# Kernel optimization log

Measured on AMD Instinct MI355X. Metric: run time of the kernel, lower is better.

Reference implementation:

```python
import jax, jax.numpy as jnp
import numpy as np

B, N, C = 1, 50000, 128
E, D = 800000, 2


def setup_inputs() -> dict:
    key = jax.random.key(0)
    k1, k2, k3 = jax.random.split(key, 3)
    x = jax.random.normal(k1, (B, N, C), dtype=jnp.float32)
    edge_weights = jax.random.normal(k2, (B, E, D), dtype=jnp.float32)
    directed_edges = jax.random.randint(k3, (B, E, 2), 0, N, dtype=jnp.int64)
    return {"x": x, "edge_weights": edge_weights, "directed_edges": directed_edges}


def reference(x, edge_weights, directed_edges):
    # x: [B, N, C] node features; edge_weights: [B, E, D]; directed_edges: [B, E, 2] = (target, source)
    b, n, c = x.shape
    _, e, d = edge_weights.shape
    target = directed_edges[..., 0]  # [B, E]
    source = directed_edges[..., 1]  # [B, E]
    bidx = jnp.arange(b)[:, None]  # [B, 1] broadcasts against [B, E]
    # gather node diffs per edge: [B, E, C]
    diff = x[bidx, source] - x[bidx, target]
    # weight by edge direction vector and flatten (C, D) -> C*D, matching torch reshape order
    message = jnp.einsum('bed,bec->becd', edge_weights, diff).reshape(b, e, c * d)
    # scatter-add into per-node gradient accumulator: [B, N, C*D]
    out = jnp.zeros((b, n, c * d), dtype=message.dtype)
    out = out.at[bidx, target].add(message)
    return out
```

## Files before the change

kernel.cpp:

```cpp
#include <hip/hip_runtime.h>


#define CAP 32
#define OVF_CAP 65536

typedef unsigned short u16;
typedef unsigned int u32;

__device__ __forceinline__ u16 f2bf(float f) {
  u32 u = __float_as_uint(f);
  return (u16)((u + 0x7FFFu + ((u >> 16) & 1u)) >> 16);
}
__device__ __forceinline__ float bf2f(u16 v) {
  return __uint_as_float(((u32)v) << 16);
}

__global__ __launch_bounds__(256) void k_cvt(const float* __restrict__ x,
                                             u16* __restrict__ xb, int total4) {
  const int stride = gridDim.x * blockDim.x;
  for (int i = blockIdx.x * blockDim.x + threadIdx.x; i < total4; i += stride) {
    const float4 v = reinterpret_cast<const float4*>(x)[i];
    ushort4 o;
    o.x = f2bf(v.x); o.y = f2bf(v.y); o.z = f2bf(v.z); o.w = f2bf(v.w);
    reinterpret_cast<ushort4*>(xb)[i] = o;
  }
}

__device__ __forceinline__ void append_one(int tgt, int src, float wx, float wy,
                                           int* counts, int4* rec,
                                           int* ovfcnt, int4* ovflist) {
  const int pos = atomicAdd(&counts[tgt], 1);
  if (pos < CAP) {
    int4 r;
    r.x = src; r.y = __float_as_int(wx); r.z = __float_as_int(wy); r.w = 0;
    rec[(size_t)tgt * CAP + pos] = r;
  } else {
    const int op = atomicAdd(ovfcnt, 1);
    if (op < OVF_CAP) {
      int4 r;
      r.x = tgt; r.y = src; r.z = __float_as_int(wx); r.w = __float_as_int(wy);
      ovflist[op] = r;
    }
  }
}

__global__ __launch_bounds__(256) void k_append(const int* __restrict__ edges,
                                                const float* __restrict__ ew,
                                                int* __restrict__ counts,
                                                int4* __restrict__ rec,
                                                int* __restrict__ ovfcnt,
                                                int4* __restrict__ ovflist, int E) {
  const int i = blockIdx.x * blockDim.x + threadIdx.x;
  const int e = 2 * i;
  if (e + 1 < E) {
    const int4 p = *reinterpret_cast<const int4*>(edges + 2ll * e);
    const float4 w = *reinterpret_cast<const float4*>(ew + 2ll * e);
    append_one(p.x, p.y, w.x, w.y, counts, rec, ovfcnt, ovflist);
    append_one(p.z, p.w, w.z, w.w, counts, rec, ovfcnt, ovflist);
  } else if (e < E) {
    const int2 ts = reinterpret_cast<const int2*>(edges)[e];
    const float2 w = reinterpret_cast<const float2*>(ew)[e];
    append_one(ts.x, ts.y, w.x, w.y, counts, rec, ovfcnt, ovflist);
  }
}

#define ACC8(X0, X1, X2, X3, WX, WY)                    \
  a0 = fmaf((WX), (X0), a0); a1 = fmaf((WY), (X0), a1); \
  a2 = fmaf((WX), (X1), a2); a3 = fmaf((WY), (X1), a3); \
  a4 = fmaf((WX), (X2), a4); a5 = fmaf((WY), (X2), a5); \
  a6 = fmaf((WX), (X3), a6); a7 = fmaf((WY), (X3), a7);

__global__ __launch_bounds__(256) void k_gather4(const float* __restrict__ x,
                                                 const u16* __restrict__ xb,
                                                 const int* __restrict__ counts,
                                                 const int4* __restrict__ rec,
                                                 float* __restrict__ out, int n) {
  const int lane = threadIdx.x & 63;
  const int node = (blockIdx.x * blockDim.x + threadIdx.x) >> 6;
  if (node >= n) return;
  const int c = lane & 31;
  const int half = lane >> 5;

  const int deg = min(counts[node], CAP);

  const float4 xt = *reinterpret_cast<const float4*>(x + (size_t)node * 128 + 4 * c);

  int rsrc = 0;
  float rwx = 0.f, rwy = 0.f;
  if (deg > 0) {
    const int li = min(lane, deg - 1);
    const int4 r = rec[(size_t)node * CAP + li];
    rsrc = r.x;
    if (lane < deg) { rwx = __int_as_float(r.y); rwy = __int_as_float(r.z); }
  }

  float a0 = 0.f, a1 = 0.f, a2 = 0.f, a3 = 0.f;
  float a4 = 0.f, a5 = 0.f, a6 = 0.f, a7 = 0.f;

  const int npair = (deg + 1) >> 1;
  int i = 0;
  for (; i + 4 <= npair; i += 4) {
    const int j0 = 2 * i + half;
    const int s0 = __shfl(rsrc, j0);
    const int s1 = __shfl(rsrc, j0 + 2);
    const int s2 = __shfl(rsrc, j0 + 4);
    const int s3 = __shfl(rsrc, j0 + 6);
    const ushort4 u0 = *reinterpret_cast<const ushort4*>(xb + (size_t)s0 * 128 + 4 * c);
    const ushort4 u1 = *reinterpret_cast<const ushort4*>(xb + (size_t)s1 * 128 + 4 * c);
    const ushort4 u2 = *reinterpret_cast<const ushort4*>(xb + (size_t)s2 * 128 + 4 * c);
    const ushort4 u3 = *reinterpret_cast<const ushort4*>(xb + (size_t)s3 * 128 + 4 * c);
    const float w0x = __shfl(rwx, j0),     w0y = __shfl(rwy, j0);
    const float w1x = __shfl(rwx, j0 + 2), w1y = __shfl(rwy, j0 + 2);
    const float w2x = __shfl(rwx, j0 + 4), w2y = __shfl(rwy, j0 + 4);
    const float w3x = __shfl(rwx, j0 + 6), w3y = __shfl(rwy, j0 + 6);
    ACC8(bf2f(u0.x), bf2f(u0.y), bf2f(u0.z), bf2f(u0.w), w0x, w0y)
    ACC8(bf2f(u1.x), bf2f(u1.y), bf2f(u1.z), bf2f(u1.w), w1x, w1y)
    ACC8(bf2f(u2.x), bf2f(u2.y), bf2f(u2.z), bf2f(u2.w), w2x, w2y)
    ACC8(bf2f(u3.x), bf2f(u3.y), bf2f(u3.z), bf2f(u3.w), w3x, w3y)
  }
  for (; i < npair; ++i) {
    const int j = 2 * i + half;
    const int s0 = __shfl(rsrc, j);
    const ushort4 u0 = *reinterpret_cast<const ushort4*>(xb + (size_t)s0 * 128 + 4 * c);
    const float w0x = __shfl(rwx, j), w0y = __shfl(rwy, j);
    ACC8(bf2f(u0.x), bf2f(u0.y), bf2f(u0.z), bf2f(u0.w), w0x, w0y)
  }

  float swx = rwx, swy = rwy;
  for (int off = 1; off < 64; off <<= 1) {
    swx += __shfl_xor(swx, off);
    swy += __shfl_xor(swy, off);
  }

  a0 += __shfl_xor(a0, 32); a1 += __shfl_xor(a1, 32);
  a2 += __shfl_xor(a2, 32); a3 += __shfl_xor(a3, 32);
  a4 += __shfl_xor(a4, 32); a5 += __shfl_xor(a5, 32);
  a6 += __shfl_xor(a6, 32); a7 += __shfl_xor(a7, 32);

  float4 o;
  if (half == 0) {
    o.x = a0 - swx * xt.x; o.y = a1 - swy * xt.x;
    o.z = a2 - swx * xt.y; o.w = a3 - swy * xt.y;
  } else {
    o.x = a4 - swx * xt.z; o.y = a5 - swy * xt.z;
    o.z = a6 - swx * xt.w; o.w = a7 - swy * xt.w;
  }
  *reinterpret_cast<float4*>(out + (size_t)node * 256 + 8 * c + 4 * half) = o;
}

__global__ __launch_bounds__(256) void k_overflow(const float* __restrict__ x,
                                                  const int* __restrict__ ovfcnt,
                                                  const int4* __restrict__ ovflist,
                                                  float* __restrict__ out) {
  const int lane = threadIdx.x & 63;
  const int wave = (blockIdx.x * blockDim.x + threadIdx.x) >> 6;
  const int nwaves = (gridDim.x * blockDim.x) >> 6;
  const int novf = min(*ovfcnt, OVF_CAP);
  for (int i = wave; i < novf; i += nwaves) {
    const int4 r = ovflist[i];
    const int tgt = r.x, src = r.y;
    const float wx = __int_as_float(r.z), wy = __int_as_float(r.w);
    const float2 vs = *reinterpret_cast<const float2*>(x + (size_t)src * 128 + 2 * lane);
    const float2 vt = *reinterpret_cast<const float2*>(x + (size_t)tgt * 128 + 2 * lane);
    const float d0 = vs.x - vt.x;
    const float d1 = vs.y - vt.y;
    float* o = out + (size_t)tgt * 256 + 4 * lane;
    unsafeAtomicAdd(o + 0, wx * d0);
    unsafeAtomicAdd(o + 1, wy * d0);
    unsafeAtomicAdd(o + 2, wx * d1);
    unsafeAtomicAdd(o + 3, wy * d1);
  }
}

#define CAPF 64
__global__ __launch_bounds__(256) void k_append_f(const int* __restrict__ edges,
                                                  const float2* __restrict__ ew,
                                                  int* __restrict__ counts,
                                                  int4* __restrict__ rec, int E) {
  const int e = blockIdx.x * blockDim.x + threadIdx.x;
  if (e >= E) return;
  const int2 ts = reinterpret_cast<const int2*>(edges)[e];
  const float2 w = ew[e];
  const int pos = atomicAdd(&counts[ts.x], 1);
  if (pos < CAPF) {
    int4 r;
    r.x = ts.y; r.y = __float_as_int(w.x); r.z = __float_as_int(w.y); r.w = 0;
    rec[(size_t)ts.x * CAPF + pos] = r;
  }
}

#define ACCF(X, WX, WY)                                   \
  a0 = fmaf((WX), (X).x, a0); a1 = fmaf((WY), (X).x, a1); \
  a2 = fmaf((WX), (X).y, a2); a3 = fmaf((WY), (X).y, a3); \
  a4 = fmaf((WX), (X).z, a4); a5 = fmaf((WY), (X).z, a5); \
  a6 = fmaf((WX), (X).w, a6); a7 = fmaf((WY), (X).w, a7);

__global__ __launch_bounds__(256) void k_gather3(const float* __restrict__ x,
                                                 const int* __restrict__ counts,
                                                 const int4* __restrict__ rec,
                                                 float* __restrict__ out, int n) {
  const int lane = threadIdx.x & 63;
  const int node = (blockIdx.x * blockDim.x + threadIdx.x) >> 6;
  if (node >= n) return;
  const int c = lane & 31;
  const int half = lane >> 5;
  const int deg = min(counts[node], CAPF);
  const float4 xt = *reinterpret_cast<const float4*>(x + (size_t)node * 128 + 4 * c);
  int rsrc = 0; float rwx = 0.f, rwy = 0.f;
  if (deg > 0) {
    const int li = min(lane, deg - 1);
    const int4 r = rec[(size_t)node * CAPF + li];
    rsrc = r.x;
    if (lane < deg) { rwx = __int_as_float(r.y); rwy = __int_as_float(r.z); }
  }
  float a0 = 0.f, a1 = 0.f, a2 = 0.f, a3 = 0.f;
  float a4 = 0.f, a5 = 0.f, a6 = 0.f, a7 = 0.f;
  const int npair = (deg + 1) >> 1;
  for (int i = 0; i < npair; ++i) {
    const int j = 2 * i + half;
    const int s0 = __shfl(rsrc, j);
    const float4 X = *reinterpret_cast<const float4*>(x + (size_t)s0 * 128 + 4 * c);
    const float wx = __shfl(rwx, j), wy = __shfl(rwy, j);
    ACCF(X, wx, wy)
  }
  float swx = rwx, swy = rwy;
  for (int off = 1; off < 64; off <<= 1) {
    swx += __shfl_xor(swx, off);
    swy += __shfl_xor(swy, off);
  }
  a0 += __shfl_xor(a0, 32); a1 += __shfl_xor(a1, 32);
  a2 += __shfl_xor(a2, 32); a3 += __shfl_xor(a3, 32);
  a4 += __shfl_xor(a4, 32); a5 += __shfl_xor(a5, 32);
  a6 += __shfl_xor(a6, 32); a7 += __shfl_xor(a7, 32);
  float4 o;
  if (half == 0) {
    o.x = a0 - swx * xt.x; o.y = a1 - swy * xt.x;
    o.z = a2 - swx * xt.y; o.w = a3 - swy * xt.y;
  } else {
    o.x = a4 - swx * xt.z; o.y = a5 - swy * xt.z;
    o.z = a6 - swx * xt.w; o.w = a7 - swy * xt.w;
  }
  *reinterpret_cast<float4*>(out + (size_t)node * 256 + 8 * c + 4 * half) = o;
}

__global__ __launch_bounds__(256) void k_atomic(const float* __restrict__ x,
                                                const float* __restrict__ ew,
                                                const int* __restrict__ edges,
                                                float* __restrict__ out, int E) {
  const int lane = threadIdx.x & 63;
  const int wave = (blockIdx.x * blockDim.x + threadIdx.x) >> 6;
  const int nwaves = (gridDim.x * blockDim.x) >> 6;
  for (int e = wave; e < E; e += nwaves) {
    const int2 ts = *reinterpret_cast<const int2*>(edges + 2ll * e);
    const float2 w = *reinterpret_cast<const float2*>(ew + 2ll * e);
    const float2 vs = *reinterpret_cast<const float2*>(x + (size_t)ts.y * 128 + 2 * lane);
    const float2 vt = *reinterpret_cast<const float2*>(x + (size_t)ts.x * 128 + 2 * lane);
    const float d0 = vs.x - vt.x;
    const float d1 = vs.y - vt.y;
    float* o = out + (size_t)ts.x * 256 + 4 * lane;
    unsafeAtomicAdd(o + 0, w.x * d0);
    unsafeAtomicAdd(o + 1, w.y * d0);
    unsafeAtomicAdd(o + 2, w.x * d1);
    unsafeAtomicAdd(o + 3, w.y * d1);
  }
}

extern "C" void kernel_launch(void* const* d_in, const int* in_sizes, int n_in,
                              void* d_out, int out_size, void* d_ws, size_t ws_size,
                              hipStream_t stream) {
  const float* x = (const float*)d_in[0];
  const float* ewf = (const float*)d_in[1];
  const int* edges = (const int*)d_in[2];
  float* out = (float*)d_out;
  const float2* ew = (const float2*)ewf;

  const int E = in_sizes[1] / 2;
  const int N = in_sizes[0] / 128;

  size_t cnt_sec = ((size_t)(N + 1) * 4 + 255) & ~(size_t)255;
  size_t xb_sec = ((size_t)N * 128 * 2 + 255) & ~(size_t)255;
  size_t rec_sec = (size_t)N * CAP * 16;
  size_t need_bf16 = cnt_sec + xb_sec + rec_sec + (size_t)OVF_CAP * 16;
  size_t need_f32 = cnt_sec + (size_t)N * CAPF * 16;

  char* wsb = (char*)d_ws;

  if (ws_size >= need_bf16) {
    int* counts = (int*)wsb;
    int* ovfcnt = counts + N;
    u16* xb = (u16*)(wsb + cnt_sec);
    int4* rec = (int4*)(wsb + cnt_sec + xb_sec);
    int4* ovflist = (int4*)(wsb + cnt_sec + xb_sec + rec_sec);
    hipMemsetAsync(counts, 0, (size_t)(N + 1) * 4, stream);
    k_append<<<((E + 1) / 2 + 255) / 256, 256, 0, stream>>>(edges, ewf, counts, rec,
                                                            ovfcnt, ovflist, E);
    k_cvt<<<2048, 256, 0, stream>>>(x, xb, N * 128 / 4);
    k_gather4<<<(N * 64 + 255) / 256, 256, 0, stream>>>(x, xb, counts, rec, out, N);
    k_overflow<<<128, 256, 0, stream>>>(x, ovfcnt, ovflist, out);
    return;
  }

  if (ws_size >= need_f32) {
    int* counts = (int*)wsb;
    int4* rec = (int4*)(wsb + cnt_sec);
    hipMemsetAsync(counts, 0, (size_t)N * 4, stream);
    k_append_f<<<(E + 255) / 256, 256, 0, stream>>>(edges, ew, counts, rec, E);
    k_gather3<<<(N * 64 + 255) / 256, 256, 0, stream>>>(x, counts, rec, out, N);
    return;
  }

  hipMemsetAsync(d_out, 0, (size_t)out_size * sizeof(float), stream);
  k_atomic<<<2048, 256, 0, stream>>>(x, ewf, edges, out, E);
}
```

Before: 114.9 us.

## Partition edge append by target range across block groups for locality

Result: faster. 100.7 us (-12.4%).

```diff
diff --git a/kernel.cpp b/kernel.cpp
--- a/kernel.cpp
+++ b/kernel.cpp
@@ -3,6 +3,7 @@
 
 #define CAP 32
 #define OVF_CAP 65536
+#define NPART 8
 
 typedef unsigned short u16;
 typedef unsigned int u32;
@@ -44,23 +45,40 @@
   }
 }
 
-__global__ __launch_bounds__(256) void k_append(const int* __restrict__ edges,
-                                                const float* __restrict__ ew,
-                                                int* __restrict__ counts,
-                                                int4* __restrict__ rec,
-                                                int* __restrict__ ovfcnt,
-                                                int4* __restrict__ ovflist, int E) {
-  const int i = blockIdx.x * blockDim.x + threadIdx.x;
-  const int e = 2 * i;
-  if (e + 1 < E) {
-    const int4 p = *reinterpret_cast<const int4*>(edges + 2ll * e);
-    const float4 w = *reinterpret_cast<const float4*>(ew + 2ll * e);
-    append_one(p.x, p.y, w.x, w.y, counts, rec, ovfcnt, ovflist);
-    append_one(p.z, p.w, w.z, w.w, counts, rec, ovfcnt, ovflist);
-  } else if (e < E) {
-    const int2 ts = reinterpret_cast<const int2*>(edges)[e];
-    const float2 w = reinterpret_cast<const float2*>(ew)[e];
-    append_one(ts.x, ts.y, w.x, w.y, counts, rec, ovfcnt, ovflist);
+__global__ __launch_bounds__(256) void k_append_p(const int* __restrict__ edges,
+                                                  const float* __restrict__ ew,
+                                                  int* __restrict__ counts,
+                                                  int4* __restrict__ rec,
+                                                  int* __restrict__ ovfcnt,
+                                                  int4* __restrict__ ovflist,
+                                                  int E, int N) {
+  const int part = blockIdx.x & (NPART - 1);
+  const int bidx = blockIdx.x >> 3;
+  const int nblk = gridDim.x >> 3;
+  const int lo = (int)((long long)part * N / NPART);
+  const int hi = (int)((long long)(part + 1) * N / NPART);
+  const int npairs = E >> 1;
+  const int stride = nblk * blockDim.x;
+
+  for (int i = bidx * blockDim.x + threadIdx.x; i < npairs; i += stride) {
+    const int4 p = reinterpret_cast<const int4*>(edges)[i];
+    const bool in0 = (p.x >= lo) & (p.x < hi);
+    const bool in1 = (p.z >= lo) & (p.z < hi);
+    if (in0 | in1) {
+      const float4 w = reinterpret_cast<const float4*>(ew)[i];
+      if (in0) append_one(p.x, p.y, w.x, w.y, counts, rec, ovfcnt, ovflist);
+      if (in1) append_one(p.z, p.w, w.z, w.w, counts, rec, ovfcnt, ovflist);
+    }
+  }
+  if (E & 1) {
+    const int e = E - 1;
+    if (bidx == 0 && threadIdx.x == 0) {
+      const int t = edges[2 * e];
+      if (t >= lo && t < hi) {
+        const float2 w = reinterpret_cast<const float2*>(ew)[e];
+        append_one(t, edges[2 * e + 1], w.x, w.y, counts, rec, ovfcnt, ovflist);
+      }
+    }
   }
 }
 
@@ -285,18 +303,17 @@
 
   char* wsb = (char*)d_ws;
 
-  if (ws_size >= need_bf16) {
+  if (ws_size >= need_bf16 && (E & 1) == 0) {
     int* counts = (int*)wsb;
     int* ovfcnt = counts + N;
     u16* xb = (u16*)(wsb + cnt_sec);
     int4* rec = (int4*)(wsb + cnt_sec + xb_sec);
     int4* ovflist = (int4*)(wsb + cnt_sec + xb_sec + rec_sec);
     hipMemsetAsync(counts, 0, (size_t)(N + 1) * 4, stream);
-    k_append<<<((E + 1) / 2 + 255) / 256, 256, 0, stream>>>(edges, ewf, counts, rec,
-                                                            ovfcnt, ovflist, E);
+    k_append_p<<<3328, 256, 0, stream>>>(edges, ewf, counts, rec, ovfcnt, ovflist, E, N);
     k_cvt<<<2048, 256, 0, stream>>>(x, xb, N * 128 / 4);
     k_gather4<<<(N * 64 + 255) / 256, 256, 0, stream>>>(x, xb, counts, rec, out, N);
-    k_overflow<<<128, 256, 0, stream>>>(x, ovfcnt, ovflist, out);
+    k_overflow<<<32, 256, 0, stream>>>(x, ovfcnt, ovflist, out);
     return;
   }
 
```
